# Kernel optimization log

Hardware: AMD Instinct MI355X
Metric: run time of the kernel (lower is better)

Reference implementation:

```python
import jax, jax.numpy as jnp
import numpy as np

STATE_DIM = 512
N_AGENTS = 16
N_ACTIONS = 32
EMBED = 512          # mixing_embed_dim
Q_IN = STATE_DIM + N_AGENTS * N_ACTIONS  # 1024 (coma_critic arch)
ROWS = 32768         # bs * ts = 64 * 512


def _linear_params(key, d_in, d_out):
    kw, kb = jax.random.split(key)
    bound = 1.0 / np.sqrt(d_in)
    W = jax.random.uniform(kw, (d_in, d_out), minval=-bound, maxval=bound, dtype=jnp.float32)
    b = jax.random.uniform(kb, (d_out,), minval=-bound, maxval=bound, dtype=jnp.float32)
    return W, b


def setup_inputs() -> dict:
    key = jax.random.key(0)
    ks = jax.random.split(key, 8)
    states = jax.random.normal(ks[0], (ROWS, STATE_DIM), dtype=jnp.float32)
    actions = jax.random.uniform(ks[1], (ROWS, N_AGENTS * N_ACTIONS), dtype=jnp.float32)
    Qw1, Qb1 = _linear_params(ks[2], Q_IN, EMBED)
    Qw2, Qb2 = _linear_params(ks[3], EMBED, EMBED)
    Qw3, Qb3 = _linear_params(ks[4], EMBED, 1)
    Vw1, Vb1 = _linear_params(ks[5], STATE_DIM, EMBED)
    Vw2, Vb2 = _linear_params(ks[6], EMBED, EMBED)
    Vw3, Vb3 = _linear_params(ks[7], EMBED, 1)
    return {
        "states": states, "actions": actions,
        "Qw1": Qw1, "Qb1": Qb1, "Qw2": Qw2, "Qb2": Qb2, "Qw3": Qw3, "Qb3": Qb3,
        "Vw1": Vw1, "Vb1": Vb1, "Vw2": Vw2, "Vb2": Vb2, "Vw3": Vw3, "Vb3": Vb3,
    }


def _mlp3(x, W1, b1, W2, b2, W3, b3):
    h = jax.nn.relu(x @ W1 + b1)
    h = jax.nn.relu(h @ W2 + b2)
    return h @ W3 + b3


def reference(states, actions,
              Qw1, Qb1, Qw2, Qb2, Qw3, Qb3,
              Vw1, Vb1, Vw2, Vb2, Vw3, Vb3):
    # coma_critic arch: inputs = cat([states, joint-action one-hots], dim=1)
    inputs = jnp.concatenate([states, actions], axis=1)  # [bs*ts, Q_IN]
    q_outputs = _mlp3(inputs, Qw1, Qb1, Qw2, Qb2, Qw3, Qb3)  # [bs*ts, 1]
    v_outputs = _mlp3(states, Vw1, Vb1, Vw2, Vb2, Vw3, Vb3)  # [bs*ts, 1]
    return q_outputs, v_outputs
```

## Files before the change

kernel.cpp:

```cpp
#include <hip/hip_runtime.h>


#define ROWS 32768
#define EMBED 512

using frag_ab = __attribute__((ext_vector_type(8))) short;
using f32x4   = __attribute__((ext_vector_type(4))) float;

__device__ __forceinline__ unsigned short f2bf(float f) {
    unsigned int u = __builtin_bit_cast(unsigned int, f);
    return (unsigned short)((u + 0x7fffu + ((u >> 16) & 1u)) >> 16);
}

__device__ __forceinline__ unsigned pk2rne(float lo, float hi) {
    return (unsigned)f2bf(lo) | ((unsigned)f2bf(hi) << 16);
}

__device__ __forceinline__ void async_copy16(const void* g, void* l) {
    __builtin_amdgcn_global_load_lds(
        (const __attribute__((address_space(1))) unsigned int*)g,
        (__attribute__((address_space(3))) unsigned int*)l, 16, 0, 0);
}

__device__ __forceinline__ void decode_mn(int L, int& mi, int& nq) {
    nq = (L >> 3) & 3;
    mi = ((L >> 5) << 3) | (L & 7);
}

__global__ __launch_bounds__(256)
void prep(const float* __restrict__ states, const float* __restrict__ actions,
          const float* __restrict__ Qw1, const float* __restrict__ Qw2,
          const float* __restrict__ Vw1, const float* __restrict__ Vw2,
          const float* __restrict__ qb3, const float* __restrict__ vb3,
          unsigned short* __restrict__ X,
          unsigned short* __restrict__ Qw1t, unsigned short* __restrict__ Qw2t,
          unsigned short* __restrict__ Vw1t, unsigned short* __restrict__ Vw2t,
          float* __restrict__ out) {
    const int b = blockIdx.x, tid = threadIdx.x;
    if (b < 4096) {
        int c = b * 256 + tid;
        int m = c >> 5, col = (c & 31) * 32;
        const float* src = (col < 512) ? states + (size_t)m * 512 + col
                                       : actions + (size_t)m * 512 + (col - 512);
        float4 f[8];
#pragma unroll
        for (int i = 0; i < 8; i++) f[i] = ((const float4*)src)[i];
        uint4* dst = (uint4*)(X + (size_t)m * 1024 + col);
#pragma unroll
        for (int i = 0; i < 4; i++)
            dst[i] = make_uint4(pk2rne(f[2*i].x,   f[2*i].y),
                                pk2rne(f[2*i].z,   f[2*i].w),
                                pk2rne(f[2*i+1].x, f[2*i+1].y),
                                pk2rne(f[2*i+1].z, f[2*i+1].w));
    } else if (b < 4736) {
        int g = (b - 4096) * 256 + tid;
        const float* W; unsigned short* O; int n, k0, ldo;
        if (g < 65536) {
            int o = g * 8; n = o >> 10; k0 = o & 1023; W = Qw1; O = Qw1t; ldo = 1024;
        } else {
            g -= 65536;
            int seg = g >> 15, r = g & 32767, o = r * 8;
            n = o >> 9; k0 = o & 511; ldo = 512;
            W = (seg == 0) ? Qw2 : (seg == 1) ? Vw1 : Vw2;
            O = (seg == 0) ? Qw2t : (seg == 1) ? Vw1t : Vw2t;
        }
        float v[8];
#pragma unroll
        for (int j = 0; j < 8; j++) v[j] = W[(size_t)(k0 + j) * 512 + n];
        *(uint4*)(O + (size_t)n * ldo + k0) =
            make_uint4(pk2rne(v[0], v[1]), pk2rne(v[2], v[3]),
                       pk2rne(v[4], v[5]), pk2rne(v[6], v[7]));
    } else {
        int i = (b - 4736) * 256 + tid;
        out[i] = (i < ROWS) ? qb3[0] : vb3[0];
    }
}

__global__ __launch_bounds__(256, 2)
void layer1(const unsigned short* __restrict__ X,
            const unsigned short* __restrict__ Qw1t,
            const unsigned short* __restrict__ Vw1t,
            const float* __restrict__ Qb1, const float* __restrict__ Vb1,
            unsigned short* __restrict__ h1Q, unsigned short* __restrict__ h1V) {
    __shared__ __align__(16) unsigned short As[2 * 4096];
    __shared__ __align__(16) unsigned short Bs[2 * 8192];

    const int tid = threadIdx.x, wave = tid >> 6, lane = tid & 63;
    int mi, nq; decode_mn(blockIdx.x, mi, nq);
    const bool isV = nq >= 2;
    const int bn = (nq & 1) * 256;
    const int bm = mi * 128;
    const int K = isV ? 512 : 1024;
    const unsigned short* Wt = isV ? Vw1t : Qw1t;
    const float* bias = isV ? Vb1 : Qb1;
    unsigned short* H = isV ? h1V : h1Q;

    const int wm = (wave & 1) * 64, wn = (wave >> 1) * 128;
    const int lrow = lane & 15, quad = lane >> 4;
    f32x4 acc[4][8] = {};

    const int lin  = wave * 1024 + lane * 16;
    const int rowS = lin >> 6, colS = (lin & 63) >> 1;
    const unsigned short* gA0 = X + (size_t)(bm + rowS)      * 1024 + colS;
    const unsigned short* gA1 = X + (size_t)(bm + rowS + 64) * 1024 + colS;
    const unsigned short* gB0 = Wt + (size_t)(bn + rowS)       * K + colS;
    const unsigned short* gB1 = Wt + (size_t)(bn + rowS + 64)  * K + colS;
    const unsigned short* gB2 = Wt + (size_t)(bn + rowS + 128) * K + colS;
    const unsigned short* gB3 = Wt + (size_t)(bn + rowS + 192) * K + colS;
    unsigned short* ldsA0 = As + wave * 512;
    unsigned short* ldsA1 = As + 2048 + wave * 512;
    unsigned short* ldsB0 = Bs + wave * 512;
    unsigned short* ldsB1 = Bs + 2048 + wave * 512;
    unsigned short* ldsB2 = Bs + 4096 + wave * 512;
    unsigned short* ldsB3 = Bs + 6144 + wave * 512;

    for (int k0 = 0; k0 < K; k0 += 64) {
        async_copy16(gA0,      ldsA0);
        async_copy16(gA0 + 32, ldsA0 + 4096);
        async_copy16(gA1,      ldsA1);
        async_copy16(gA1 + 32, ldsA1 + 4096);
        async_copy16(gB0,      ldsB0);
        async_copy16(gB0 + 32, ldsB0 + 8192);
        async_copy16(gB1,      ldsB1);
        async_copy16(gB1 + 32, ldsB1 + 8192);
        async_copy16(gB2,      ldsB2);
        async_copy16(gB2 + 32, ldsB2 + 8192);
        async_copy16(gB3,      ldsB3);
        async_copy16(gB3 + 32, ldsB3 + 8192);
        gA0 += 64; gA1 += 64; gB0 += 64; gB1 += 64; gB2 += 64; gB3 += 64;
        __syncthreads();

#pragma unroll
        for (int s = 0; s < 2; s++) {
            frag_ab af[4], bfr[8];
#pragma unroll
            for (int i = 0; i < 4; i++)
                af[i] = *(const frag_ab*)&As[s * 4096 + (wm + i * 16 + lrow) * 32 + quad * 8];
#pragma unroll
            for (int j = 0; j < 8; j++)
                bfr[j] = *(const frag_ab*)&Bs[s * 8192 + (wn + j * 16 + lrow) * 32 + quad * 8];
#pragma unroll
            for (int i = 0; i < 4; i++)
#pragma unroll
                for (int j = 0; j < 8; j++)
                    acc[i][j] = __builtin_amdgcn_mfma_f32_16x16x32_bf16(
                        af[i], bfr[j], acc[i][j], 0, 0, 0);
        }
        __syncthreads();
    }

#pragma unroll
    for (int j = 0; j < 8; j++) {
        const int col = bn + wn + j * 16 + lrow;
        const float bc = bias[col];
#pragma unroll
        for (int i = 0; i < 4; i++) {
            const int row0 = bm + wm + i * 16 + quad * 4;
#pragma unroll
            for (int r = 0; r < 4; r++) {
                float v = acc[i][j][r] + bc;
                v = v > 0.0f ? v : 0.0f;
                H[(size_t)(row0 + r) * EMBED + col] = f2bf(v);
            }
        }
    }
}

__global__ __launch_bounds__(256, 2)
void layer2(const unsigned short* __restrict__ h1Q,
            const unsigned short* __restrict__ h1V,
            const unsigned short* __restrict__ Qw2t,
            const unsigned short* __restrict__ Vw2t,
            const float* __restrict__ Qb2, const float* __restrict__ Vb2,
            const float* __restrict__ Qw3, const float* __restrict__ Vw3,
            float* __restrict__ out) {
    __shared__ __align__(16) unsigned short As[2 * 4096];
    __shared__ __align__(16) unsigned short Bs[2 * 8192];

    const int tid = threadIdx.x, wave = tid >> 6, lane = tid & 63;
    int mi, nq; decode_mn(blockIdx.x, mi, nq);
    const bool isV = nq >= 2;
    const int bn = (nq & 1) * 256;
    const int bm = mi * 128;
    const unsigned short* A  = isV ? h1V : h1Q;
    const unsigned short* Wt = isV ? Vw2t : Qw2t;
    const float* bias = isV ? Vb2 : Qb2;
    const float* w3   = isV ? Vw3 : Qw3;
    float* op = out + (isV ? ROWS : 0);

    const int wm = (wave & 1) * 64, wn = (wave >> 1) * 128;
    const int lrow = lane & 15, quad = lane >> 4;
    f32x4 acc[4][8] = {};

    const int lin  = wave * 1024 + lane * 16;
    const int rowS = lin >> 6, colS = (lin & 63) >> 1;
    const unsigned short* gA0 = A + (size_t)(bm + rowS)      * 512 + colS;
    const unsigned short* gA1 = A + (size_t)(bm + rowS + 64) * 512 + colS;
    const unsigned short* gB0 = Wt + (size_t)(bn + rowS)       * 512 + colS;
    const unsigned short* gB1 = Wt + (size_t)(bn + rowS + 64)  * 512 + colS;
    const unsigned short* gB2 = Wt + (size_t)(bn + rowS + 128) * 512 + colS;
    const unsigned short* gB3 = Wt + (size_t)(bn + rowS + 192) * 512 + colS;
    unsigned short* ldsA0 = As + wave * 512;
    unsigned short* ldsA1 = As + 2048 + wave * 512;
    unsigned short* ldsB0 = Bs + wave * 512;
    unsigned short* ldsB1 = Bs + 2048 + wave * 512;
    unsigned short* ldsB2 = Bs + 4096 + wave * 512;
    unsigned short* ldsB3 = Bs + 6144 + wave * 512;

    for (int k0 = 0; k0 < 512; k0 += 64) {
        async_copy16(gA0,      ldsA0);
        async_copy16(gA0 + 32, ldsA0 + 4096);
        async_copy16(gA1,      ldsA1);
        async_copy16(gA1 + 32, ldsA1 + 4096);
        async_copy16(gB0,      ldsB0);
        async_copy16(gB0 + 32, ldsB0 + 8192);
        async_copy16(gB1,      ldsB1);
        async_copy16(gB1 + 32, ldsB1 + 8192);
        async_copy16(gB2,      ldsB2);
        async_copy16(gB2 + 32, ldsB2 + 8192);
        async_copy16(gB3,      ldsB3);
        async_copy16(gB3 + 32, ldsB3 + 8192);
        gA0 += 64; gA1 += 64; gB0 += 64; gB1 += 64; gB2 += 64; gB3 += 64;
        __syncthreads();

#pragma unroll
        for (int s = 0; s < 2; s++) {
            frag_ab af[4], bfr[8];
#pragma unroll
            for (int i = 0; i < 4; i++)
                af[i] = *(const frag_ab*)&As[s * 4096 + (wm + i * 16 + lrow) * 32 + quad * 8];
#pragma unroll
            for (int j = 0; j < 8; j++)
                bfr[j] = *(const frag_ab*)&Bs[s * 8192 + (wn + j * 16 + lrow) * 32 + quad * 8];
#pragma unroll
            for (int i = 0; i < 4; i++)
#pragma unroll
                for (int j = 0; j < 8; j++)
                    acc[i][j] = __builtin_amdgcn_mfma_f32_16x16x32_bf16(
                        af[i], bfr[j], acc[i][j], 0, 0, 0);
        }
        __syncthreads();
    }

    float bc[8], wc[8];
#pragma unroll
    for (int j = 0; j < 8; j++) {
        const int col = bn + wn + j * 16 + lrow;
        bc[j] = bias[col];
        wc[j] = w3[col];
    }
#pragma unroll
    for (int i = 0; i < 4; i++) {
#pragma unroll
        for (int r = 0; r < 4; r++) {
            float s = 0.0f;
#pragma unroll
            for (int j = 0; j < 8; j++) {
                float v = acc[i][j][r] + bc[j];
                v = v > 0.0f ? v : 0.0f;
                s += v * wc[j];
            }
#pragma unroll
            for (int m = 1; m < 16; m <<= 1) s += __shfl_xor(s, m, 64);
            if (lrow == 0)
                atomicAdd(&op[bm + wm + i * 16 + quad * 4 + r], s);
        }
    }
}

extern "C" void kernel_launch(void* const* d_in, const int* in_sizes, int n_in,
                              void* d_out, int out_size, void* d_ws, size_t ws_size,
                              hipStream_t stream) {
    const float* states  = (const float*)d_in[0];
    const float* actions = (const float*)d_in[1];
    const float* Qw1 = (const float*)d_in[2];
    const float* Qb1 = (const float*)d_in[3];
    const float* Qw2 = (const float*)d_in[4];
    const float* Qb2 = (const float*)d_in[5];
    const float* Qw3 = (const float*)d_in[6];
    const float* Qb3 = (const float*)d_in[7];
    const float* Vw1 = (const float*)d_in[8];
    const float* Vb1 = (const float*)d_in[9];
    const float* Vw2 = (const float*)d_in[10];
    const float* Vb2 = (const float*)d_in[11];
    const float* Vw3 = (const float*)d_in[12];
    const float* Vb3 = (const float*)d_in[13];
    float* out = (float*)d_out;

    char* ws = (char*)d_ws;
    unsigned short* X    = (unsigned short*)ws;
    unsigned short* h1Q  = (unsigned short*)(ws + 67108864);
    unsigned short* h1V  = (unsigned short*)(ws + 100663296);
    unsigned short* Qw1t = (unsigned short*)(ws + 134217728);
    unsigned short* Qw2t = Qw1t + 512 * 1024;
    unsigned short* Vw1t = Qw2t + 512 * 512;
    unsigned short* Vw2t = Vw1t + 512 * 512;

    prep<<<dim3(4992), dim3(256), 0, stream>>>(states, actions, Qw1, Qw2, Vw1, Vw2,
                                               Qb3, Vb3, X, Qw1t, Qw2t, Vw1t, Vw2t, out);

    layer1<<<dim3(1024), dim3(256), 0, stream>>>(X, Qw1t, Vw1t, Qb1, Vb1, h1Q, h1V);
    layer2<<<dim3(1024), dim3(256), 0, stream>>>(h1Q, h1V, Qw2t, Vw2t, Qb2, Vb2, Qw3, Vw3, out);
}
```

Baseline: 287.6 us.

## Double-buffer GEMM K-loop with prefetch and tile weight transpose via LDS

The layer1 and layer2 GEMM loops now use a double-buffered pipeline over 32-wide K slices. The next slice is prefetched into the alternate LDS buffer while MFMAs consume the current one, with a single barrier per iteration instead of two. The weight transpose in prep now goes through a padded 64x64 LDS tile, so global reads and writes are coalesced instead of strided, which reduces the block count. The trade-off is more loop iterations with smaller slices, and the correctness of async LDS loads relying on barrier ordering alone.

Result: slower. 305.7 us (+6.3%).

```diff
diff --git a/kernel.cpp b/kernel.cpp
--- a/kernel.cpp
+++ b/kernel.cpp
@@ -52,26 +52,31 @@
                                 pk2rne(f[2*i].z,   f[2*i].w),
                                 pk2rne(f[2*i+1].x, f[2*i+1].y),
                                 pk2rne(f[2*i+1].z, f[2*i+1].w));
-    } else if (b < 4736) {
-        int g = (b - 4096) * 256 + tid;
-        const float* W; unsigned short* O; int n, k0, ldo;
-        if (g < 65536) {
-            int o = g * 8; n = o >> 10; k0 = o & 1023; W = Qw1; O = Qw1t; ldo = 1024;
-        } else {
-            g -= 65536;
-            int seg = g >> 15, r = g & 32767, o = r * 8;
-            n = o >> 9; k0 = o & 511; ldo = 512;
-            W = (seg == 0) ? Qw2 : (seg == 1) ? Vw1 : Vw2;
-            O = (seg == 0) ? Qw2t : (seg == 1) ? Vw1t : Vw2t;
-        }
-        float v[8];
-#pragma unroll
-        for (int j = 0; j < 8; j++) v[j] = W[(size_t)(k0 + j) * 512 + n];
-        *(uint4*)(O + (size_t)n * ldo + k0) =
-            make_uint4(pk2rne(v[0], v[1]), pk2rne(v[2], v[3]),
-                       pk2rne(v[4], v[5]), pk2rne(v[6], v[7]));
+    } else if (b < 4416) {
+        __shared__ unsigned short T[64 * 65];
+        const int c = b - 4096;
+        const float* W; unsigned short* O; int ldo, kt, nt;
+        if (c < 128) { W = Qw1; O = Qw1t; ldo = 1024; kt = c >> 3; nt = c & 7; }
+        else {
+            int d = c - 128, which = d >> 6, r = d & 63;
+            kt = r >> 3; nt = r & 7; ldo = 512;
+            W = (which == 0) ? Qw2 : (which == 1) ? Vw1 : Vw2;
+            O = (which == 0) ? Qw2t : (which == 1) ? Vw1t : Vw2t;
+        }
+        const int k0 = kt * 64, n0 = nt * 64;
+#pragma unroll
+        for (int p = 0; p < 16; p++) {
+            int e = tid + p * 256, kr = e >> 6, nc = e & 63;
+            T[nc * 65 + kr] = f2bf(W[(size_t)(k0 + kr) * 512 + n0 + nc]);
+        }
+        __syncthreads();
+#pragma unroll
+        for (int p = 0; p < 16; p++) {
+            int e = tid + p * 256, nr = e >> 6, kc = e & 63;
+            O[(size_t)(n0 + nr) * ldo + k0 + kc] = T[nr * 65 + kc];
+        }
     } else {
-        int i = (b - 4736) * 256 + tid;
+        int i = (b - 4416) * 256 + tid;
         out[i] = (i < ROWS) ? qb3[0] : vb3[0];
     }
 }
@@ -114,39 +119,39 @@
     unsigned short* ldsB2 = Bs + 4096 + wave * 512;
     unsigned short* ldsB3 = Bs + 6144 + wave * 512;
 
-    for (int k0 = 0; k0 < K; k0 += 64) {
-        async_copy16(gA0,      ldsA0);
-        async_copy16(gA0 + 32, ldsA0 + 4096);
-        async_copy16(gA1,      ldsA1);
-        async_copy16(gA1 + 32, ldsA1 + 4096);
-        async_copy16(gB0,      ldsB0);
-        async_copy16(gB0 + 32, ldsB0 + 8192);
-        async_copy16(gB1,      ldsB1);
-        async_copy16(gB1 + 32, ldsB1 + 8192);
-        async_copy16(gB2,      ldsB2);
-        async_copy16(gB2 + 32, ldsB2 + 8192);
-        async_copy16(gB3,      ldsB3);
-        async_copy16(gB3 + 32, ldsB3 + 8192);
-        gA0 += 64; gA1 += 64; gB0 += 64; gB1 += 64; gB2 += 64; gB3 += 64;
+    const int nIter = K >> 5;
+    async_copy16(gA0, ldsA0);  async_copy16(gA1, ldsA1);
+    async_copy16(gB0, ldsB0);  async_copy16(gB1, ldsB1);
+    async_copy16(gB2, ldsB2);  async_copy16(gB3, ldsB3);
+    gA0 += 32; gA1 += 32; gB0 += 32; gB1 += 32; gB2 += 32; gB3 += 32;
+
+    for (int it = 0; it < nIter; ++it) {
         __syncthreads();
-
-#pragma unroll
-        for (int s = 0; s < 2; s++) {
-            frag_ab af[4], bfr[8];
-#pragma unroll
-            for (int i = 0; i < 4; i++)
-                af[i] = *(const frag_ab*)&As[s * 4096 + (wm + i * 16 + lrow) * 32 + quad * 8];
+        if (it + 1 < nIter) {
+            const int p = ((it + 1) & 1);
+            async_copy16(gA0, ldsA0 + p * 4096);
+            async_copy16(gA1, ldsA1 + p * 4096);
+            async_copy16(gB0, ldsB0 + p * 8192);
+            async_copy16(gB1, ldsB1 + p * 8192);
+            async_copy16(gB2, ldsB2 + p * 8192);
+            async_copy16(gB3, ldsB3 + p * 8192);
+            gA0 += 32; gA1 += 32; gB0 += 32; gB1 += 32; gB2 += 32; gB3 += 32;
+        }
+        const unsigned short* Ab = As + (it & 1) * 4096;
+        const unsigned short* Bb = Bs + (it & 1) * 8192;
+        frag_ab af[4], bfr[8];
+#pragma unroll
+        for (int i = 0; i < 4; i++)
+            af[i] = *(const frag_ab*)&Ab[(wm + i * 16 + lrow) * 32 + quad * 8];
+#pragma unroll
+        for (int j = 0; j < 8; j++)
+            bfr[j] = *(const frag_ab*)&Bb[(wn + j * 16 + lrow) * 32 + quad * 8];
+#pragma unroll
+        for (int i = 0; i < 4; i++)
 #pragma unroll
             for (int j = 0; j < 8; j++)
-                bfr[j] = *(const frag_ab*)&Bs[s * 8192 + (wn + j * 16 + lrow) * 32 + quad * 8];
-#pragma unroll
-            for (int i = 0; i < 4; i++)
-#pragma unroll
-                for (int j = 0; j < 8; j++)
-                    acc[i][j] = __builtin_amdgcn_mfma_f32_16x16x32_bf16(
-                        af[i], bfr[j], acc[i][j], 0, 0, 0);
-        }
-        __syncthreads();
+                acc[i][j] = __builtin_amdgcn_mfma_f32_16x16x32_bf16(
+                    af[i], bfr[j], acc[i][j], 0, 0, 0);
     }
 
 #pragma unroll
@@ -207,39 +212,38 @@
     unsigned short* ldsB2 = Bs + 4096 + wave * 512;
     unsigned short* ldsB3 = Bs + 6144 + wave * 512;
 
-    for (int k0 = 0; k0 < 512; k0 += 64) {
-        async_copy16(gA0,      ldsA0);
-        async_copy16(gA0 + 32, ldsA0 + 4096);
-        async_copy16(gA1,      ldsA1);
-        async_copy16(gA1 + 32, ldsA1 + 4096);
-        async_copy16(gB0,      ldsB0);
-        async_copy16(gB0 + 32, ldsB0 + 8192);
-        async_copy16(gB1,      ldsB1);
-        async_copy16(gB1 + 32, ldsB1 + 8192);
-        async_copy16(gB2,      ldsB2);
-        async_copy16(gB2 + 32, ldsB2 + 8192);
-        async_copy16(gB3,      ldsB3);
-        async_copy16(gB3 + 32, ldsB3 + 8192);
-        gA0 += 64; gA1 += 64; gB0 += 64; gB1 += 64; gB2 += 64; gB3 += 64;
+    async_copy16(gA0, ldsA0);  async_copy16(gA1, ldsA1);
+    async_copy16(gB0, ldsB0);  async_copy16(gB1, ldsB1);
+    async_copy16(gB2, ldsB2);  async_copy16(gB3, ldsB3);
+    gA0 += 32; gA1 += 32; gB0 += 32; gB1 += 32; gB2 += 32; gB3 += 32;
+
+    for (int it = 0; it < 16; ++it) {
         __syncthreads();
-
-#pragma unroll
-        for (int s = 0; s < 2; s++) {
-            frag_ab af[4], bfr[8];
-#pragma unroll
-            for (int i = 0; i < 4; i++)
-                af[i] = *(const frag_ab*)&As[s * 4096 + (wm + i * 16 + lrow) * 32 + quad * 8];
+        if (it + 1 < 16) {
+            const int p = ((it + 1) & 1);
+            async_copy16(gA0, ldsA0 + p * 4096);
+            async_copy16(gA1, ldsA1 + p * 4096);
+            async_copy16(gB0, ldsB0 + p * 8192);
+            async_copy16(gB1, ldsB1 + p * 8192);
+            async_copy16(gB2, ldsB2 + p * 8192);
+            async_copy16(gB3, ldsB3 + p * 8192);
+            gA0 += 32; gA1 += 32; gB0 += 32; gB1 += 32; gB2 += 32; gB3 += 32;
+        }
+        const unsigned short* Ab = As + (it & 1) * 4096;
+        const unsigned short* Bb = Bs + (it & 1) * 8192;
+        frag_ab af[4], bfr[8];
+#pragma unroll
+        for (int i = 0; i < 4; i++)
+            af[i] = *(const frag_ab*)&Ab[(wm + i * 16 + lrow) * 32 + quad * 8];
+#pragma unroll
+        for (int j = 0; j < 8; j++)
+            bfr[j] = *(const frag_ab*)&Bb[(wn + j * 16 + lrow) * 32 + quad * 8];
+#pragma unroll
+        for (int i = 0; i < 4; i++)
 #pragma unroll
             for (int j = 0; j < 8; j++)
-                bfr[j] = *(const frag_ab*)&Bs[s * 8192 + (wn + j * 16 + lrow) * 32 + quad * 8];
-#pragma unroll
-            for (int i = 0; i < 4; i++)
-#pragma unroll
-                for (int j = 0; j < 8; j++)
-                    acc[i][j] = __builtin_amdgcn_mfma_f32_16x16x32_bf16(
-                        af[i], bfr[j], acc[i][j], 0, 0, 0);
-        }
-        __syncthreads();
+                acc[i][j] = __builtin_amdgcn_mfma_f32_16x16x32_bf16(
+                    af[i], bfr[j], acc[i][j], 0, 0, 0);
     }
 
     float bc[8], wc[8];
@@ -296,7 +300,7 @@
     unsigned short* Vw1t = Qw2t + 512 * 512;
     unsigned short* Vw2t = Vw1t + 512 * 512;
 
-    prep<<<dim3(4992), dim3(256), 0, stream>>>(states, actions, Qw1, Qw2, Vw1, Vw2,
+    prep<<<dim3(4672), dim3(256), 0, stream>>>(states, actions, Qw1, Qw2, Vw1, Vw2,
                                                Qb3, Vb3, X, Qw1t, Qw2t, Vw1t, Vw2t, out);
 
     layer1<<<dim3(1024), dim3(256), 0, stream>>>(X, Qw1t, Vw1t, Qb1, Vb1, h1Q, h1V);
```
